# Performance work log

Hardware: AMD Instinct MI355X
Metric: run time of the kernel (lower is better)

The kernel has to match this reference:

```python
import jax, jax.numpy as jnp
import numpy as np

K = 3; STRIDE = 1; PAD = 1; DIL = 1  # from init_kwargs, groups=1


def setup_inputs() -> dict:
    key = jax.random.key(0)
    k1, k2, k3, k4, k5 = jax.random.split(key, 5)
    x = jax.random.normal(k1, (4, 64, 128, 128), dtype=jnp.float32)
    # small offset-conv weights so predicted offsets stay in a realistic few-pixel range
    w_off = jax.random.normal(k2, (2 * K * K, 64, K, K), dtype=jnp.float32) * 0.01
    b_off = jax.random.normal(k3, (2 * K * K,), dtype=jnp.float32) * 0.01
    w = jax.random.normal(k4, (64, 64, K, K), dtype=jnp.float32) * (1.0 / np.sqrt(64 * K * K))
    b = jax.random.normal(k5, (64,), dtype=jnp.float32) * 0.01
    return {"x": x, "w_off": w_off, "b_off": b_off, "w": w, "b": b}


def _conv2d(x, w, b):
    out = jax.lax.conv_general_dilated(
        x, w, window_strides=(STRIDE, STRIDE), padding=((PAD, PAD), (PAD, PAD)),
        rhs_dilation=(DIL, DIL), dimension_numbers=("NCHW", "OIHW", "NCHW"))
    return out + b[None, :, None, None]


def _deform_sample(x, oy, ox):
    # x: [B,C,H,W]; oy/ox: [B,K2,Ho,Wo] learned offsets (y,x)
    B, C, H, W = x.shape
    K2, Ho, Wo = oy.shape[1], oy.shape[2], oy.shape[3]
    k_idx = jnp.arange(K2)
    kh = (k_idx // K).astype(jnp.float32)
    kw = (k_idx % K).astype(jnp.float32)
    base_y = kh[:, None] * DIL + (jnp.arange(Ho, dtype=jnp.float32) * STRIDE - PAD)[None, :]  # [K2,Ho]
    base_x = kw[:, None] * DIL + (jnp.arange(Wo, dtype=jnp.float32) * STRIDE - PAD)[None, :]  # [K2,Wo]
    y = base_y[None, :, :, None] + oy  # [B,K2,Ho,Wo]
    xp = base_x[None, :, None, :] + ox
    y0f = jnp.floor(y); x0f = jnp.floor(xp)
    wy = y - y0f; wx = xp - x0f
    y0 = y0f.astype(jnp.int32); x0 = x0f.astype(jnp.int32)
    imgf = x.reshape(B, C, H * W)
    N = K2 * Ho * Wo

    def gather(yi, xi, cw):
        valid = (yi >= 0) & (yi < H) & (xi >= 0) & (xi < W)  # zero padding outside
        yc = jnp.clip(yi, 0, H - 1); xc = jnp.clip(xi, 0, W - 1)
        idx = (yc * W + xc).reshape(B, 1, N)
        g = jnp.take_along_axis(imgf, idx, axis=2)  # [B,C,N]
        m = (cw * valid.astype(cw.dtype)).reshape(B, 1, N)
        return g * m

    acc = gather(y0, x0, (1 - wy) * (1 - wx))
    acc = acc + gather(y0, x0 + 1, (1 - wy) * wx)
    acc = acc + gather(y0 + 1, x0, wy * (1 - wx))
    acc = acc + gather(y0 + 1, x0 + 1, wy * wx)
    return acc.reshape(B, C, K2, Ho, Wo)


def reference(x, w_off, b_off, w, b):
    # offset-predicting conv (standard conv2d)
    off = _conv2d(x, w_off, b_off)  # [B, 2*K*K, Ho, Wo]
    B = off.shape[0]; Ho, Wo = off.shape[2], off.shape[3]
    off = off.reshape(B, K * K, 2, Ho, Wo)
    oy, ox = off[:, :, 0], off[:, :, 1]
    sampled = _deform_sample(x, oy, ox)  # [B,C,K2,Ho,Wo]
    O = w.shape[0]
    out = jnp.einsum("bckhw,ock->bohw", sampled, w.reshape(O, w.shape[1], K * K))
    return out + b[None, :, None, None]
```

## Files before the change

### kernel.cpp

```cpp
#include <hip/hip_runtime.h>


typedef unsigned short u16;
typedef __attribute__((ext_vector_type(8))) short bf16x8;
typedef __attribute__((ext_vector_type(4))) float f32x4;
#define MFMA __builtin_amdgcn_mfma_f32_16x16x32_bf16

__device__ __forceinline__ void bsplit(float v, u16& h, u16& l) {
  unsigned u = __float_as_uint(v);
  unsigned hb = (u + 0x7fffu + ((u >> 16) & 1u)) & 0xffff0000u;
  h = (u16)(hb >> 16);
  float r = v - __uint_as_float(hb);
  unsigned u2 = __float_as_uint(r);
  l = (u16)((u2 + 0x7fffu + ((u2 >> 16) & 1u)) >> 16);
}

__global__ __launch_bounds__(256) void prep_weights(
    const float* __restrict__ w, const float* __restrict__ w_off,
    u16* __restrict__ whi, u16* __restrict__ wlo,
    u16* __restrict__ wofh, u16* __restrict__ wofl) {
  int t = blockIdx.x * 256 + threadIdx.x;
  int stride = gridDim.x * 256;
  for (int i = t; i < 9 * 64 * 64; i += stride) {
    int tap = i >> 12, o = (i >> 6) & 63, c = i & 63;
    u16 h, l;
    bsplit(w[o * 576 + c * 9 + tap], h, l);
    whi[i] = h; wlo[i] = l;
  }
  for (int i = t; i < 9 * 32 * 64; i += stride) {
    int tap = i >> 11, ch = (i >> 6) & 31, c = i & 63;
    float v = (ch < 18) ? w_off[ch * 576 + c * 9 + tap] : 0.f;
    u16 h, l;
    bsplit(v, h, l);
    wofh[i] = h; wofl[i] = l;
  }
}

__global__ __launch_bounds__(256) void transpose_x(
    const float* __restrict__ x, float* __restrict__ xt) {
  __shared__ float tile[64][65];
  int blk = blockIdx.x;
  int wchunk = blk & 1;
  int h = (blk >> 1) & 127;
  int b = blk >> 8;
  int w0 = wchunk * 64;
  int r = threadIdx.x >> 6;
  int lane = threadIdx.x & 63;
#pragma unroll
  for (int i = 0; i < 16; i++) {
    int c = r + i * 4;
    tile[c][lane] = x[(((size_t)(b * 64 + c) * 128) + h) * 128 + w0 + lane];
  }
  __syncthreads();
#pragma unroll
  for (int i = 0; i < 16; i++) {
    int wi = r + i * 4;
    xt[(((size_t)(b * 128 + h) * 128) + w0 + wi) * 64 + lane] = tile[lane][wi];
  }
}

__global__ __launch_bounds__(256) void offset_conv(
    const float* __restrict__ xt, const u16* __restrict__ wofh,
    const u16* __restrict__ wofl, const float* __restrict__ b_off,
    float* __restrict__ off_pix) {
  int blk = blockIdx.x;
  int hp = blk & 63, b = blk >> 6;
  int h0 = hp * 2;
  int lane = threadIdx.x & 63, wv = threadIdx.x >> 6;
  int lm = lane & 15, lg = lane >> 4;
  const float* xb = xt + (size_t)b * (128 * 128 * 64);

  f32x4 acc[4][2];
#pragma unroll
  for (int i = 0; i < 4; i++)
#pragma unroll
    for (int j = 0; j < 2; j++) acc[i][j] = (f32x4)0.f;

#pragma unroll 1
  for (int tap = 0; tap < 9; tap++) {
    int ky = tap / 3, kx = tap - ky * 3;
#pragma unroll
    for (int kc = 0; kc < 2; kc++) {
      const u16* ah = wofh + tap * 2048 + lm * 64 + kc * 32 + lg * 8;
      const u16* al = wofl + tap * 2048 + lm * 64 + kc * 32 + lg * 8;
      bf16x8 a0h = *(const bf16x8*)ah;
      bf16x8 a0l = *(const bf16x8*)al;
      bf16x8 a1h = *(const bf16x8*)(ah + 1024);
      bf16x8 a1l = *(const bf16x8*)(al + 1024);
#pragma unroll
      for (int pt = 0; pt < 4; pt++) {
        int y = h0 + (pt >> 1) + ky - 1;
        if ((unsigned)y >= 128u) continue;
        int xx = wv * 32 + (pt & 1) * 16 + lm + kx - 1;
        bool valid = (unsigned)xx < 128u;
        int xc = min(max(xx, 0), 127);
        const float* xp = xb + ((size_t)(y * 128 + xc)) * 64 + kc * 32 + lg * 8;
        float4 xa = *(const float4*)xp;
        float4 xc4 = *(const float4*)(xp + 4);
        if (!valid) { xa = make_float4(0, 0, 0, 0); xc4 = make_float4(0, 0, 0, 0); }
        bf16x8 bh, bl;
        u16 h, l;
        bsplit(xa.x, h, l); bh[0] = h; bl[0] = l;
        bsplit(xa.y, h, l); bh[1] = h; bl[1] = l;
        bsplit(xa.z, h, l); bh[2] = h; bl[2] = l;
        bsplit(xa.w, h, l); bh[3] = h; bl[3] = l;
        bsplit(xc4.x, h, l); bh[4] = h; bl[4] = l;
        bsplit(xc4.y, h, l); bh[5] = h; bl[5] = l;
        bsplit(xc4.z, h, l); bh[6] = h; bl[6] = l;
        bsplit(xc4.w, h, l); bh[7] = h; bl[7] = l;
        acc[pt][0] = MFMA(a0h, bh, acc[pt][0], 0, 0, 0);
        acc[pt][0] = MFMA(a0h, bl, acc[pt][0], 0, 0, 0);
        acc[pt][0] = MFMA(a0l, bh, acc[pt][0], 0, 0, 0);
        acc[pt][1] = MFMA(a1h, bh, acc[pt][1], 0, 0, 0);
        acc[pt][1] = MFMA(a1h, bl, acc[pt][1], 0, 0, 0);
        acc[pt][1] = MFMA(a1l, bh, acc[pt][1], 0, 0, 0);
      }
    }
  }

  float4 bo = *(const float4*)(b_off + 4 * lg);
  float b16 = b_off[16], b17 = b_off[17];
#pragma unroll
  for (int pt = 0; pt < 4; pt++) {
    int y = h0 + (pt >> 1);
    int wc = wv * 32 + (pt & 1) * 16 + lm;
    size_t base = ((size_t)((b * 128 + y) * 128) + wc) * 18;
    float2 s0 = make_float2(acc[pt][0][0] + bo.x, acc[pt][0][1] + bo.y);
    float2 s1 = make_float2(acc[pt][0][2] + bo.z, acc[pt][0][3] + bo.w);
    *(float2*)(off_pix + base + 4 * lg) = s0;
    *(float2*)(off_pix + base + 4 * lg + 2) = s1;
    if (lg == 0) {
      float2 s2 = make_float2(acc[pt][1][0] + b16, acc[pt][1][1] + b17);
      *(float2*)(off_pix + base + 16) = s2;
    }
  }
}

#define SWZ(p, byt) ((byt) ^ (((p) & 7) << 4))
__global__ __launch_bounds__(256) void dcn_main(
    const float* __restrict__ xt, const float* __restrict__ off_pix,
    const u16* __restrict__ whi, const u16* __restrict__ wlo,
    const float* __restrict__ bias, float* __restrict__ out) {
  __shared__ __align__(16) float coef[576 * 8];
  __shared__ __align__(16) u16 shi[64 * 64];
  __shared__ __align__(16) u16 slo[64 * 64];

  int blk = blockIdx.x;
  int wc = blk & 1, h = (blk >> 1) & 127, b = blk >> 8;
  int w0 = wc * 64;
  int tid = threadIdx.x, lane = tid & 63, wave = tid >> 6;
  int lm = lane & 15, lg = lane >> 4;
  const float* xbase = xt + (size_t)b * (128 * 128 * 64);
  const float* offbase = off_pix + (size_t)((b * 128 + h) * 128 + w0) * 18;

  for (int it = tid; it < 576; it += 256) {
    int p = it / 9, k = it - p * 9;
    int ky = k / 3, kx = k - ky * 3;
    float2 o2 = *reinterpret_cast<const float2*>(offbase + p * 18 + 2 * k);
    float yf = (float)(h + ky - 1) + o2.x;
    float xf = (float)(w0 + p + kx - 1) + o2.y;
    float y0f = floorf(yf), x0f = floorf(xf);
    float wy = yf - y0f, wx = xf - x0f;
    int y0 = (int)y0f, x0 = (int)x0f;
    int y1 = y0 + 1, x1 = x0 + 1;
    float w00 = (1.f - wy) * (1.f - wx);
    float w01 = (1.f - wy) * wx;
    float w10 = wy * (1.f - wx);
    float w11 = wy * wx;
    bool vy0 = (unsigned)y0 < 128u, vy1 = (unsigned)y1 < 128u;
    bool vx0 = (unsigned)x0 < 128u, vx1 = (unsigned)x1 < 128u;
    if (!(vy0 && vx0)) w00 = 0.f;
    if (!(vy0 && vx1)) w01 = 0.f;
    if (!(vy1 && vx0)) w10 = 0.f;
    if (!(vy1 && vx1)) w11 = 0.f;
    int y0c = min(max(y0, 0), 127), y1c = min(max(y1, 0), 127);
    int x0c = min(max(x0, 0), 127), x1c = min(max(x1, 0), 127);
    float* cp = &coef[it * 8];
    *reinterpret_cast<float4*>(cp) = make_float4(w00, w01, w10, w11);
    *reinterpret_cast<int4*>(cp + 4) =
        make_int4((y0c * 128 + x0c) * 64, (y0c * 128 + x1c) * 64,
                  (y1c * 128 + x0c) * 64, (y1c * 128 + x1c) * 64);
  }

  f32x4 acc[4];
#pragma unroll
  for (int i = 0; i < 4; i++) acc[i] = (f32x4)0.f;

  __syncthreads();

#pragma unroll 1
  for (int tap = 0; tap < 9; tap++) {
#pragma unroll 4
    for (int i = 0; i < 16; i++) {
      int p = wave * 16 + i;
      const float* cp = &coef[(p * 9 + tap) * 8];
      float4 cw = *reinterpret_cast<const float4*>(cp);
      int4 ci = *reinterpret_cast<const int4*>(cp + 4);
      float v = cw.x * xbase[ci.x + lane] + cw.y * xbase[ci.y + lane] +
                cw.z * xbase[ci.z + lane] + cw.w * xbase[ci.w + lane];
      u16 hb, lb;
      bsplit(v, hb, lb);
      int byt = SWZ(p, p * 128 + lane * 2);
      *(u16*)((char*)shi + byt) = hb;
      *(u16*)((char*)slo + byt) = lb;
    }
    __syncthreads();

    const u16* wh = whi + tap * 4096 + (wave * 16 + lm) * 64 + lg * 8;
    const u16* wl = wlo + tap * 4096 + (wave * 16 + lm) * 64 + lg * 8;
    bf16x8 ah0 = *(const bf16x8*)wh;
    bf16x8 ah1 = *(const bf16x8*)(wh + 32);
    bf16x8 al0 = *(const bf16x8*)wl;
    bf16x8 al1 = *(const bf16x8*)(wl + 32);

#pragma unroll
    for (int pt = 0; pt < 4; pt++) {
      int p = pt * 16 + lm;
      int byt0 = SWZ(p, p * 128 + lg * 16);
      int byt1 = SWZ(p, p * 128 + 64 + lg * 16);
      bf16x8 bh0 = *(const bf16x8*)((char*)shi + byt0);
      bf16x8 bl0 = *(const bf16x8*)((char*)slo + byt0);
      bf16x8 bh1 = *(const bf16x8*)((char*)shi + byt1);
      bf16x8 bl1 = *(const bf16x8*)((char*)slo + byt1);
      acc[pt] = MFMA(ah0, bh0, acc[pt], 0, 0, 0);
      acc[pt] = MFMA(ah0, bl0, acc[pt], 0, 0, 0);
      acc[pt] = MFMA(al0, bh0, acc[pt], 0, 0, 0);
      acc[pt] = MFMA(ah1, bh1, acc[pt], 0, 0, 0);
      acc[pt] = MFMA(ah1, bl1, acc[pt], 0, 0, 0);
      acc[pt] = MFMA(al1, bh1, acc[pt], 0, 0, 0);
    }
    __syncthreads();
  }

  float4 bv = *(const float4*)(bias + wave * 16 + 4 * lg);
#pragma unroll
  for (int pt = 0; pt < 4; pt++) {
#pragma unroll
    for (int r = 0; r < 4; r++) {
      int o = wave * 16 + 4 * lg + r;
      float bb = (r == 0) ? bv.x : (r == 1) ? bv.y : (r == 2) ? bv.z : bv.w;
      out[((size_t)(b * 64 + o)) * 16384 + h * 128 + w0 + pt * 16 + lm] =
          acc[pt][r] + bb;
    }
  }
}

extern "C" void kernel_launch(void* const* d_in, const int* in_sizes, int n_in,
                              void* d_out, int out_size, void* d_ws, size_t ws_size,
                              hipStream_t stream) {
  const float* x     = (const float*)d_in[0];
  const float* w_off = (const float*)d_in[1];
  const float* b_off = (const float*)d_in[2];
  const float* w     = (const float*)d_in[3];
  const float* b     = (const float*)d_in[4];
  float* out = (float*)d_out;
  char* ws = (char*)d_ws;

  u16*   whi     = (u16*)(ws);
  u16*   wlo     = (u16*)(ws + 73728);
  u16*   wofh    = (u16*)(ws + 147456);
  u16*   wofl    = (u16*)(ws + 184320);
  float* xt      = (float*)(ws + 221184);
  float* off_pix = (float*)(ws + 16998400);

  prep_weights<<<64, 256, 0, stream>>>(w, w_off, whi, wlo, wofh, wofl);
  transpose_x<<<1024, 256, 0, stream>>>(x, xt);
  offset_conv<<<256, 256, 0, stream>>>(xt, wofh, wofl, b_off, off_pix);
  dcn_main<<<1024, 256, 0, stream>>>(xt, off_pix, whi, wlo, b, out);
}
```

Measured before the change: 199.5 us.

## Prefetch next tap's bilinear gathers into registers and remap block order

In the deformable-conv main kernel, the 64 scattered global gathers for the next tap are issued into a 16x4 register array right after the barrier, so their latency overlaps the MFMA work of the current tap. The coefficient table is split into separate weight and index LDS arrays. Block IDs are also permuted so that eight consecutive blocks map to different image rows and batches, which changes L2 locality and CU distribution. The extra 64 live float registers per thread could lower occupancy or cause spills.

```diff
diff --git a/kernel.cpp b/kernel.cpp
--- a/kernel.cpp
+++ b/kernel.cpp
@@ -141,18 +141,21 @@
     const float* __restrict__ xt, const float* __restrict__ off_pix,
     const u16* __restrict__ whi, const u16* __restrict__ wlo,
     const float* __restrict__ bias, float* __restrict__ out) {
-  __shared__ __align__(16) float coef[576 * 8];
+  __shared__ __align__(16) float cw_lds[576][4];
+  __shared__ __align__(16) int   ci_lds[576][4];
   __shared__ __align__(16) u16 shi[64 * 64];
   __shared__ __align__(16) u16 slo[64 * 64];
 
   int blk = blockIdx.x;
-  int wc = blk & 1, h = (blk >> 1) & 127, b = blk >> 8;
+  int wg = ((blk & 7) << 7) | (blk >> 3);
+  int wc = wg & 1, h = (wg >> 1) & 127, b = wg >> 8;
   int w0 = wc * 64;
   int tid = threadIdx.x, lane = tid & 63, wave = tid >> 6;
   int lm = lane & 15, lg = lane >> 4;
   const float* xbase = xt + (size_t)b * (128 * 128 * 64);
   const float* offbase = off_pix + (size_t)((b * 128 + h) * 128 + w0) * 18;
 
+#pragma unroll 1
   for (int it = tid; it < 576; it += 256) {
     int p = it / 9, k = it - p * 9;
     int ky = k / 3, kx = k - ky * 3;
@@ -175,36 +178,54 @@
     if (!(vy1 && vx1)) w11 = 0.f;
     int y0c = min(max(y0, 0), 127), y1c = min(max(y1, 0), 127);
     int x0c = min(max(x0, 0), 127), x1c = min(max(x1, 0), 127);
-    float* cp = &coef[it * 8];
-    *reinterpret_cast<float4*>(cp) = make_float4(w00, w01, w10, w11);
-    *reinterpret_cast<int4*>(cp + 4) =
+    *(float4*)cw_lds[it] = make_float4(w00, w01, w10, w11);
+    *(int4*)ci_lds[it] =
         make_int4((y0c * 128 + x0c) * 64, (y0c * 128 + x1c) * 64,
                   (y1c * 128 + x0c) * 64, (y1c * 128 + x1c) * 64);
   }
+  __syncthreads();
 
   f32x4 acc[4];
 #pragma unroll
   for (int i = 0; i < 4; i++) acc[i] = (f32x4)0.f;
 
-  __syncthreads();
+  float g[16][4];
+
+#pragma unroll
+  for (int i = 0; i < 16; i++) {
+    int4 ci = *(const int4*)ci_lds[(wave * 16 + i) * 9 + 0];
+    g[i][0] = xbase[ci.x + lane];
+    g[i][1] = xbase[ci.y + lane];
+    g[i][2] = xbase[ci.z + lane];
+    g[i][3] = xbase[ci.w + lane];
+  }
 
 #pragma unroll 1
   for (int tap = 0; tap < 9; tap++) {
-#pragma unroll 4
+#pragma unroll
     for (int i = 0; i < 16; i++) {
       int p = wave * 16 + i;
-      const float* cp = &coef[(p * 9 + tap) * 8];
-      float4 cw = *reinterpret_cast<const float4*>(cp);
-      int4 ci = *reinterpret_cast<const int4*>(cp + 4);
-      float v = cw.x * xbase[ci.x + lane] + cw.y * xbase[ci.y + lane] +
-                cw.z * xbase[ci.z + lane] + cw.w * xbase[ci.w + lane];
-      u16 hb, lb;
-      bsplit(v, hb, lb);
+      float4 cwv = *(const float4*)cw_lds[p * 9 + tap];
+      float v = cwv.x * g[i][0] + cwv.y * g[i][1] +
+                cwv.z * g[i][2] + cwv.w * g[i][3];
+      u16 hh, ll;
+      bsplit(v, hh, ll);
       int byt = SWZ(p, p * 128 + lane * 2);
-      *(u16*)((char*)shi + byt) = hb;
-      *(u16*)((char*)slo + byt) = lb;
+      *(u16*)((char*)shi + byt) = hh;
+      *(u16*)((char*)slo + byt) = ll;
     }
     __syncthreads();
+
+    if (tap < 8) {
+#pragma unroll
+      for (int i = 0; i < 16; i++) {
+        int4 ci = *(const int4*)ci_lds[(wave * 16 + i) * 9 + tap + 1];
+        g[i][0] = xbase[ci.x + lane];
+        g[i][1] = xbase[ci.y + lane];
+        g[i][2] = xbase[ci.z + lane];
+        g[i][3] = xbase[ci.w + lane];
+      }
+    }
 
     const u16* wh = whi + tap * 4096 + (wave * 16 + lm) * 64 + lg * 8;
     const u16* wl = wlo + tap * 4096 + (wave * 16 + lm) * 64 + lg * 8;
@@ -212,7 +233,6 @@
     bf16x8 ah1 = *(const bf16x8*)(wh + 32);
     bf16x8 al0 = *(const bf16x8*)wl;
     bf16x8 al1 = *(const bf16x8*)(wl + 32);
-
 #pragma unroll
     for (int pt = 0; pt < 4; pt++) {
       int p = pt * 16 + lm;
@@ -233,14 +253,13 @@
   }
 
   float4 bv = *(const float4*)(bias + wave * 16 + 4 * lg);
+  size_t ob = ((size_t)(b * 64 + wave * 16 + 4 * lg)) * 16384 + h * 128 + w0;
 #pragma unroll
   for (int pt = 0; pt < 4; pt++) {
 #pragma unroll
     for (int r = 0; r < 4; r++) {
-      int o = wave * 16 + 4 * lg + r;
       float bb = (r == 0) ? bv.x : (r == 1) ? bv.y : (r == 2) ? bv.z : bv.w;
-      out[((size_t)(b * 64 + o)) * 16384 + h * 128 + w0 + pt * 16 + lm] =
-          acc[pt][r] + bb;
+      out[ob + (size_t)r * 16384 + pt * 16 + lm] = acc[pt][r] + bb;
     }
   }
 }
@@ -260,11 +279,11 @@
   u16*   wlo     = (u16*)(ws + 73728);
   u16*   wofh    = (u16*)(ws + 147456);
   u16*   wofl    = (u16*)(ws + 184320);
-  float* xt      = (float*)(ws + 221184);
+  float* xtw     = (float*)(ws + 221184);
   float* off_pix = (float*)(ws + 16998400);
 
   prep_weights<<<64, 256, 0, stream>>>(w, w_off, whi, wlo, wofh, wofl);
-  transpose_x<<<1024, 256, 0, stream>>>(x, xt);
-  offset_conv<<<256, 256, 0, stream>>>(xt, wofh, wofl, b_off, off_pix);
-  dcn_main<<<1024, 256, 0, stream>>>(xt, off_pix, whi, wlo, b, out);
-}
+  transpose_x<<<1024, 256, 0, stream>>>(x, xtw);
+  offset_conv<<<256, 256, 0, stream>>>(xtw, wofh, wofl, b_off, off_pix);
+  dcn_main<<<1024, 256, 0, stream>>>(xtw, off_pix, whi, wlo, b, out);
+}
```

Result: faster. 174.1 us (-12.7%).
